# Kernel optimization log

Hardware: AMD Instinct MI355X
Metric: run time of the kernel (lower is better)

## Reference

```python
import jax, jax.numpy as jnp
import numpy as np

B, T, C = 8, 4096, 256
N_LAYER, LAYER_ID = 12, 5


def setup_inputs() -> dict:
    key = jax.random.key(0)
    ks = jax.random.split(key, 5)
    x = jax.random.normal(ks[0], (B, T, C), dtype=jnp.float32)
    scale = 1.0 / np.sqrt(C)
    Wk = jax.random.normal(ks[1], (C, C), jnp.float32) * scale
    Wv = jax.random.normal(ks[2], (C, C), jnp.float32) * scale
    Wr = jax.random.normal(ks[3], (C, C), jnp.float32) * scale
    Wo = jax.random.normal(ks[4], (C, C), jnp.float32) * scale
    # 'fancy' init from _init_weights
    ratio_0_to_1 = LAYER_ID / (N_LAYER - 1)
    h = np.arange(C, dtype=np.float64)
    decay = -5.0 + 8.0 * (h / (C - 1)) ** (0.7 + 1.3 * ratio_0_to_1)
    zigzag = ((np.arange(C) + 1) % 3 - 1) * 0.5
    first = np.log(0.3) + zigzag
    return dict(
        x=x, Wk=Wk, Wv=Wv, Wr=Wr, Wo=Wo,
        spatial_decay=jnp.asarray(decay, jnp.float32),
        spatial_first=jnp.asarray(first, jnp.float32),
        ln_w=jnp.ones((C,), jnp.float32),
        ln_b=jnp.zeros((C,), jnp.float32),
    )


def _wkv(w, u, k, v):
    # Numerically-stable RWKV WKV scan, matching wkv_cuda forward.
    # w, u: [C] (already divided by T); k, v: [B, T, C]. Returns y: [B, T, C].
    MIN_VALUE = -1e38

    def step(carry, kv):
        p, q, o = carry            # [B, C] each
        kt, vt = kv                # [B, C]
        no = jnp.maximum(o, u + kt)
        a = jnp.exp(o - no)
        b = jnp.exp(u + kt - no)
        y = (a * p + b * vt) / (a * q + b)
        no2 = jnp.maximum(w + o, kt)
        a2 = jnp.exp(w + o - no2)
        b2 = jnp.exp(kt - no2)
        return (a2 * p + b2 * vt, a2 * q + b2, no2), y

    p0 = jnp.zeros(k.shape[0:1] + k.shape[2:3], k.dtype)  # [B, C]
    q0 = jnp.zeros_like(p0)
    o0 = jnp.full_like(p0, MIN_VALUE)
    kT = jnp.swapaxes(k, 0, 1)  # [T, B, C]
    vT = jnp.swapaxes(v, 0, 1)
    _, yT = jax.lax.scan(step, (p0, q0, o0), (kT, vT))
    return jnp.swapaxes(yT, 0, 1)


def _layernorm(x, w, b, eps=1e-5):
    mu = jnp.mean(x, axis=-1, keepdims=True)
    xc = x - mu
    var = jnp.mean(xc * xc, axis=-1, keepdims=True)
    return xc * jax.lax.rsqrt(var + eps) * w + b


def reference(x, Wk, Wv, Wr, Wo, spatial_decay, spatial_first, ln_w, ln_b):
    # shift_pixel == 0 -> xk = xv = xr = x (module's own code path)
    t = x.shape[1]
    k = jnp.einsum('btc,dc->btd', x, Wk)
    v = jnp.einsum('btc,dc->btd', x, Wv)
    r = jnp.einsum('btc,dc->btd', x, Wr)
    sr = jax.nn.sigmoid(r)
    y = _wkv(spatial_decay / t, spatial_first / t, k, v)
    y = _layernorm(y, ln_w, ln_b)
    return jnp.einsum('btc,dc->btd', sr * y, Wo)
```

## Files before the change

### kernel.cpp

```cpp
#include <hip/hip_runtime.h>
#include <cstdint>
#include <cstddef>

#define B_ 8
#define T_ 4096
#define C_ 256
#define NC_ 256
#define L_ (T_ / NC_)
#define M_ (B_ * T_)

typedef float f32x4 __attribute__((ext_vector_type(4)));
typedef short bf16x8 __attribute__((ext_vector_type(8)));

__device__ __forceinline__ unsigned short f2b(float f) {
    unsigned int u = __float_as_uint(f);
    u += 0x7fffu + ((u >> 16) & 1u);
    return (unsigned short)(u >> 16);
}
__device__ __forceinline__ float b2f(unsigned short h) {
    return __uint_as_float(((unsigned int)h) << 16);
}

__global__ __launch_bounds__(256) void cvt_all(const float* __restrict__ x,
                                               const float* __restrict__ Wk,
                                               const float* __restrict__ Wv,
                                               const float* __restrict__ Wr,
                                               const float* __restrict__ Wo,
                                               unsigned short* __restrict__ xb,
                                               unsigned short* __restrict__ wb) {
    const int bid = blockIdx.x;
    const float* src;
    unsigned short* dst;
    size_t base;
    if (bid < 4096) {
        src = x; dst = xb;
        base = (size_t)bid * 2048;
    } else {
        const int r = bid - 4096;
        const int mat = r >> 5;
        src = (mat == 0) ? Wk : (mat == 1) ? Wv : (mat == 2) ? Wr : Wo;
        dst = wb + (size_t)mat * 65536;
        base = (size_t)(r & 31) * 2048;
    }
    const size_t i = base + (size_t)threadIdx.x * 8;
    float4 a = *(const float4*)(src + i);
    float4 b = *(const float4*)(src + i + 4);
    bf16x8 o;
    o[0] = (short)f2b(a.x); o[1] = (short)f2b(a.y);
    o[2] = (short)f2b(a.z); o[3] = (short)f2b(a.w);
    o[4] = (short)f2b(b.x); o[5] = (short)f2b(b.y);
    o[6] = (short)f2b(b.z); o[7] = (short)f2b(b.w);
    *(bf16x8*)(dst + i) = o;
}

__global__ __launch_bounds__(256, 3) void gemm_qkv(const unsigned short* __restrict__ A,
                                                   const unsigned short* __restrict__ w0,
                                                   const unsigned short* __restrict__ w1,
                                                   const unsigned short* __restrict__ w2,
                                                   float* __restrict__ f0,
                                                   float* __restrict__ f1,
                                                   unsigned short* __restrict__ b2) {
    __shared__ unsigned short wlds[64 * 264];
    __shared__ float stage[4][16 * 68];
    const int tid = threadIdx.x;
    const int wave = tid >> 6, lane = tid & 63;
    const int quad = lane >> 4, l16 = lane & 15;
    const int m0 = blockIdx.x * 64 + wave * 16;
    const int n0 = blockIdx.y * 64;
    float* myst = stage[wave];

    bf16x8 af[8];
    {
        const unsigned short* Ar = A + (size_t)(m0 + l16) * C_ + quad * 8;
#pragma unroll
        for (int kc = 0; kc < 8; ++kc) af[kc] = *(const bf16x8*)(Ar + kc * 32);
    }

    const int r = tid >> 5;
    const int cs = (tid & 31) * 8;

    bf16x8 tmp[8];
#pragma unroll
    for (int it = 0; it < 8; ++it)
        tmp[it] = *(const bf16x8*)(w0 + (size_t)(n0 + it * 8 + r) * C_ + cs);

    for (int mat = 0; mat < 3; ++mat) {
        __syncthreads();
#pragma unroll
        for (int it = 0; it < 8; ++it)
            *(bf16x8*)(wlds + (it * 8 + r) * 264 + cs) = tmp[it];
        __syncthreads();

        if (mat < 2) {
            const unsigned short* Wn = (mat == 0) ? w1 : w2;
#pragma unroll
            for (int it = 0; it < 8; ++it)
                tmp[it] = *(const bf16x8*)(Wn + (size_t)(n0 + it * 8 + r) * C_ + cs);
        }

        f32x4 acc[4];
#pragma unroll
        for (int nt = 0; nt < 4; ++nt) acc[nt] = (f32x4){0.f, 0.f, 0.f, 0.f};
#pragma unroll
        for (int nt = 0; nt < 4; ++nt) {
            const unsigned short* wrow = wlds + (nt * 16 + l16) * 264 + quad * 8;
#pragma unroll
            for (int kc = 0; kc < 8; ++kc) {
                bf16x8 wf = *(const bf16x8*)(wrow + kc * 32);
                acc[nt] = __builtin_amdgcn_mfma_f32_16x16x32_bf16(af[kc], wf, acc[nt], 0, 0, 0);
            }
        }

#pragma unroll
        for (int nt = 0; nt < 4; ++nt)
#pragma unroll
            for (int i = 0; i < 4; ++i)
                myst[(quad * 4 + i) * 68 + nt * 16 + l16] = acc[nt][i];
#pragma unroll
        for (int rr = 0; rr < 4; ++rr) {
            const int row = rr * 4 + quad;
            float4 t4 = *(const float4*)&myst[row * 68 + l16 * 4];
            const size_t gidx = (size_t)(m0 + row) * C_ + n0 + l16 * 4;
            if (mat == 0) {
                *(float4*)(f0 + gidx) = t4;
            } else if (mat == 1) {
                *(float4*)(f1 + gidx) = t4;
            } else {
                ushort4 s4;
                s4.x = f2b(1.f / (1.f + __expf(-t4.x)));
                s4.y = f2b(1.f / (1.f + __expf(-t4.y)));
                s4.z = f2b(1.f / (1.f + __expf(-t4.z)));
                s4.w = f2b(1.f / (1.f + __expf(-t4.w)));
                *(ushort4*)(b2 + gidx) = s4;
            }
        }
    }
}

__global__ __launch_bounds__(256, 3) void gemm_out(const unsigned short* __restrict__ A,
                                                   const unsigned short* __restrict__ w0,
                                                   float* __restrict__ f0) {
    __shared__ unsigned short wlds[64 * 264];
    __shared__ float stage[4][16 * 68];
    const int tid = threadIdx.x;
    const int wave = tid >> 6, lane = tid & 63;
    const int quad = lane >> 4, l16 = lane & 15;
    const int m0 = blockIdx.x * 64 + wave * 16;
    const int n0 = blockIdx.y * 64;
    float* myst = stage[wave];

    {
        const int r = tid >> 5;
        const int cs = (tid & 31) * 8;
        bf16x8 tmp[8];
#pragma unroll
        for (int it = 0; it < 8; ++it)
            tmp[it] = *(const bf16x8*)(w0 + (size_t)(n0 + it * 8 + r) * C_ + cs);
#pragma unroll
        for (int it = 0; it < 8; ++it)
            *(bf16x8*)(wlds + (it * 8 + r) * 264 + cs) = tmp[it];
    }
    __syncthreads();

    bf16x8 af[8];
    {
        const unsigned short* Ar = A + (size_t)(m0 + l16) * C_ + quad * 8;
#pragma unroll
        for (int kc = 0; kc < 8; ++kc) af[kc] = *(const bf16x8*)(Ar + kc * 32);
    }

    f32x4 acc[4];
#pragma unroll
    for (int nt = 0; nt < 4; ++nt) acc[nt] = (f32x4){0.f, 0.f, 0.f, 0.f};
#pragma unroll
    for (int nt = 0; nt < 4; ++nt) {
        const unsigned short* wrow = wlds + (nt * 16 + l16) * 264 + quad * 8;
#pragma unroll
        for (int kc = 0; kc < 8; ++kc) {
            bf16x8 wf = *(const bf16x8*)(wrow + kc * 32);
            acc[nt] = __builtin_amdgcn_mfma_f32_16x16x32_bf16(af[kc], wf, acc[nt], 0, 0, 0);
        }
    }

#pragma unroll
    for (int nt = 0; nt < 4; ++nt)
#pragma unroll
        for (int i = 0; i < 4; ++i)
            myst[(quad * 4 + i) * 68 + nt * 16 + l16] = acc[nt][i];
#pragma unroll
    for (int rr = 0; rr < 4; ++rr) {
        const int row = rr * 4 + quad;
        float4 t4 = *(const float4*)&myst[row * 68 + l16 * 4];
        *(float4*)(f0 + (size_t)(m0 + row) * C_ + n0 + l16 * 4) = t4;
    }
}

__global__ __launch_bounds__(256) void wkv_pass1(const float* __restrict__ k,
                                                 const float* __restrict__ v,
                                                 const float* __restrict__ decay,
                                                 float* __restrict__ sp, float* __restrict__ sq,
                                                 float* __restrict__ so) {
    const int c = threadIdx.x, chunk = blockIdx.x, b = blockIdx.y;
    const float w = decay[c] * (1.0f / T_);
    size_t base = ((size_t)b * T_ + (size_t)chunk * L_) * C_ + c;
    float p = 0.f, q = 0.f, o = -1e38f;
    for (int t = 0; t < L_; t += 8) {
        float kk[8], vv[8];
#pragma unroll
        for (int j = 0; j < 8; ++j) {
            kk[j] = k[base + (size_t)(t + j) * C_];
            vv[j] = v[base + (size_t)(t + j) * C_];
        }
#pragma unroll
        for (int j = 0; j < 8; ++j) {
            float wo = w + o;
            float no = fmaxf(wo, kk[j]);
            float a2 = __expf(wo - no), b2 = __expf(kk[j] - no);
            p = a2 * p + b2 * vv[j];
            q = a2 * q + b2;
            o = no;
        }
    }
    size_t idx = ((size_t)b * NC_ + chunk) * C_ + c;
    sp[idx] = p; sq[idx] = q; so[idx] = o;
}

__global__ __launch_bounds__(256) void wkv_combine_par(const float* __restrict__ decay,
                                                       float* __restrict__ sp,
                                                       float* __restrict__ sq,
                                                       float* __restrict__ so) {
    __shared__ float tp[16][17], tq[16][17], to[16][17];
    const int tid = threadIdx.x;
    const int cg = tid >> 4;
    const int cl = tid & 15;
    const int b = blockIdx.x;
    const int c = blockIdx.y * 16 + cl;
    const float wL = decay[c] * (1.0f / T_) * (float)L_;
    const float wL16 = wL * 16.0f;
    const size_t base = ((size_t)b * NC_ + (size_t)cg * 16) * C_ + c;

    float p = 0.f, q = 0.f, o = -1e38f;
#pragma unroll 4
    for (int j = 0; j < 16; ++j) {
        size_t idx = base + (size_t)j * C_;
        float lp = sp[idx], lq = sq[idx], lo = so[idx];
        float ow = o + wL;
        float no = fmaxf(ow, lo);
        float ea = __expf(ow - no), eb = __expf(lo - no);
        p = ea * p + eb * lp;
        q = ea * q + eb * lq;
        o = no;
    }
    tp[cg][cl] = p; tq[cg][cl] = q; to[cg][cl] = o;

    float ip = p, iq = q, io = o;
#pragma unroll
    for (int off = 1; off < 16; off <<= 1) {
        __syncthreads();
        float ap = 0.f, aq = 0.f, ao = 0.f;
        const bool doit = (cg >= off);
        if (doit) { ap = tp[cg - off][cl]; aq = tq[cg - off][cl]; ao = to[cg - off][cl]; }
        __syncthreads();
        if (doit) {
            float ow = ao + (float)off * wL16;
            float no = fmaxf(ow, io);
            float ea = __expf(ow - no), eb = __expf(io - no);
            ip = ea * ap + eb * ip;
            iq = ea * aq + eb * iq;
            io = no;
            tp[cg][cl] = ip; tq[cg][cl] = iq; to[cg][cl] = io;
        }
    }
    __syncthreads();

    float ep, eq, eo;
    if (cg == 0) { ep = 0.f; eq = 0.f; eo = -1e38f; }
    else         { ep = tp[cg - 1][cl]; eq = tq[cg - 1][cl]; eo = to[cg - 1][cl]; }

    for (int j = 0; j < 16; ++j) {
        size_t idx = base + (size_t)j * C_;
        float lp = sp[idx], lq = sq[idx], lo = so[idx];
        sp[idx] = ep; sq[idx] = eq; so[idx] = eo;
        float ow = eo + wL;
        float no = fmaxf(ow, lo);
        float ea = __expf(ow - no), eb = __expf(lo - no);
        ep = ea * ep + eb * lp;
        eq = ea * eq + eb * lq;
        eo = no;
    }
}

__global__ __launch_bounds__(256, 8) void wkv_pass2_ln(const float* __restrict__ k,
                                                       const float* __restrict__ v,
                                                       const unsigned short* __restrict__ sr,
                                                       const float* __restrict__ decay,
                                                       const float* __restrict__ first,
                                                       const float* __restrict__ lw,
                                                       const float* __restrict__ lb,
                                                       const float* __restrict__ sp,
                                                       const float* __restrict__ sq,
                                                       const float* __restrict__ so,
                                                       unsigned short* __restrict__ z) {
    __shared__ float tile[16][264];
    __shared__ float mu_s[16], rs_s[16];
    const int c = threadIdx.x, chunk = blockIdx.x, b = blockIdx.y;
    const int wave = c >> 6, lane = c & 63;
    const float w = decay[c] * (1.0f / T_);
    const float u = first[c] * (1.0f / T_);
    const float gw = lw[c], gb = lb[c];
    size_t sidx = ((size_t)b * NC_ + chunk) * C_ + c;
    float p = sp[sidx], q = sq[sidx], o = so[sidx];
    size_t base = ((size_t)b * T_ + (size_t)chunk * L_) * C_ + c;

    for (int t = 0; t < L_; t += 8) {
        float kk[8], vv[8];
#pragma unroll
        for (int j = 0; j < 8; ++j) {
            kk[j] = k[base + (size_t)(t + j) * C_];
            vv[j] = v[base + (size_t)(t + j) * C_];
        }
#pragma unroll
        for (int j = 0; j < 8; ++j) {
            float uk = u + kk[j];
            float no = fmaxf(o, uk);
            float a = __expf(o - no), bb = __expf(uk - no);
            tile[t + j][c] = (a * p + bb * vv[j]) / (a * q + bb);
            float wo = w + o;
            float no2 = fmaxf(wo, kk[j]);
            float a2 = __expf(wo - no2), b2 = __expf(kk[j] - no2);
            p = a2 * p + b2 * vv[j];
            q = a2 * q + b2;
            o = no2;
        }
    }
    __syncthreads();
#pragma unroll
    for (int r = 0; r < 4; ++r) {
        const int j = wave * 4 + r;
        float4 t4 = *(const float4*)&tile[j][lane * 4];
        float s = t4.x + t4.y + t4.z + t4.w;
        float ss = t4.x * t4.x + t4.y * t4.y + t4.z * t4.z + t4.w * t4.w;
#pragma unroll
        for (int m = 1; m < 64; m <<= 1) {
            s += __shfl_xor(s, m, 64);
            ss += __shfl_xor(ss, m, 64);
        }
        if (lane == 0) {
            float mu = s * (1.f / C_);
            mu_s[j] = mu;
            rs_s[j] = rsqrtf(ss * (1.f / C_) - mu * mu + 1e-5f);
        }
    }
    __syncthreads();
#pragma unroll
    for (int j = 0; j < L_; ++j) {
        float zz = (tile[j][c] - mu_s[j]) * rs_s[j] * gw + gb;
        zz *= b2f(sr[base + (size_t)j * C_]);
        z[base + (size_t)j * C_] = f2b(zz);
    }
}

extern "C" void kernel_launch(void* const* d_in, const int* in_sizes, int n_in,
                              void* d_out, int out_size, void* d_ws, size_t ws_size,
                              hipStream_t stream) {
    const float* x     = (const float*)d_in[0];
    const float* Wk    = (const float*)d_in[1];
    const float* Wv    = (const float*)d_in[2];
    const float* Wr    = (const float*)d_in[3];
    const float* Wo    = (const float*)d_in[4];
    const float* decay = (const float*)d_in[5];
    const float* first = (const float*)d_in[6];
    const float* lnw   = (const float*)d_in[7];
    const float* lnb   = (const float*)d_in[8];
    float* out = (float*)d_out;

    char* ws = (char*)d_ws;
    const size_t NE = (size_t)M_ * C_;
    unsigned short* wb  = (unsigned short*)ws; ws += 4 * 65536 * 2;
    unsigned short* xb  = (unsigned short*)ws; ws += NE * 2;
    float* kbuf = (float*)ws; ws += NE * 4;
    float* vbuf = (float*)ws; ws += NE * 4;
    unsigned short* srb = (unsigned short*)ws; ws += NE * 2;
    unsigned short* zb  = (unsigned short*)ws; ws += NE * 2;
    const size_t SE = (size_t)B_ * NC_ * C_;
    float* sp = (float*)ws; ws += SE * 4;
    float* sq = (float*)ws; ws += SE * 4;
    float* so = (float*)ws; ws += SE * 4;
    unsigned short* wkb = wb;
    unsigned short* wvb = wb + 65536;
    unsigned short* wrb = wb + 2 * 65536;
    unsigned short* wob = wb + 3 * 65536;

    cvt_all<<<4096 + 128, 256, 0, stream>>>(x, Wk, Wv, Wr, Wo, xb, wb);

    gemm_qkv<<<dim3(M_ / 64, 4), 256, 0, stream>>>(xb, wkb, wvb, wrb,
                                                   kbuf, vbuf, srb);

    wkv_pass1<<<dim3(NC_, B_), 256, 0, stream>>>(kbuf, vbuf, decay, sp, sq, so);
    wkv_combine_par<<<dim3(B_, C_ / 16), 256, 0, stream>>>(decay, sp, sq, so);
    wkv_pass2_ln<<<dim3(NC_, B_), 256, 0, stream>>>(kbuf, vbuf, srb, decay, first,
                                                    lnw, lnb, sp, sq, so, zb);

    gemm_out<<<dim3(M_ / 64, 4), 256, 0, stream>>>(zb, wob, out);
}
```

Baseline: 171.7 us.

## Fuse WKV chunk-state pass into QKV GEMM epilogue

Each wave's 16-row by 64-channel tile of K and V, which matches one 16-step WKV chunk, is kept in registers from the LDS staging buffer. The per-chunk (p, q, o) state is then computed directly in the GEMM epilogue. This removes the separate wkv_pass1 kernel, its launch, and its re-read of the K and V buffers from global memory. In exchange it adds registers and a serial exp chain to the GEMM kernel, which may lower occupancy under launch_bounds(256,3).

```diff
diff --git a/kernel.cpp b/kernel.cpp
--- a/kernel.cpp
+++ b/kernel.cpp
@@ -57,9 +57,13 @@
                                                    const unsigned short* __restrict__ w0,
                                                    const unsigned short* __restrict__ w1,
                                                    const unsigned short* __restrict__ w2,
+                                                   const float* __restrict__ decay,
                                                    float* __restrict__ f0,
                                                    float* __restrict__ f1,
-                                                   unsigned short* __restrict__ b2) {
+                                                   unsigned short* __restrict__ b2,
+                                                   float* __restrict__ sp,
+                                                   float* __restrict__ sq,
+                                                   float* __restrict__ so) {
     __shared__ unsigned short wlds[64 * 264];
     __shared__ float stage[4][16 * 68];
     const int tid = threadIdx.x;
@@ -83,6 +87,8 @@
 #pragma unroll
     for (int it = 0; it < 8; ++it)
         tmp[it] = *(const bf16x8*)(w0 + (size_t)(n0 + it * 8 + r) * C_ + cs);
+
+    float kreg[16], vreg[16];
 
     for (int mat = 0; mat < 3; ++mat) {
         __syncthreads();
@@ -134,6 +140,30 @@
                 *(ushort4*)(b2 + gidx) = s4;
             }
         }
+
+        if (mat == 0) {
+#pragma unroll
+            for (int j = 0; j < L_; ++j) kreg[j] = myst[j * 68 + lane];
+        } else if (mat == 1) {
+#pragma unroll
+            for (int j = 0; j < L_; ++j) vreg[j] = myst[j * 68 + lane];
+            const int ch = n0 + lane;
+            const float w = decay[ch] * (1.0f / T_);
+            float p = 0.f, q = 0.f, o = -1e38f;
+#pragma unroll
+            for (int j = 0; j < L_; ++j) {
+                float wo = w + o;
+                float no = fmaxf(wo, kreg[j]);
+                float a2 = __expf(wo - no), b2s = __expf(kreg[j] - no);
+                p = a2 * p + b2s * vreg[j];
+                q = a2 * q + b2s;
+                o = no;
+            }
+            const int bb = m0 / T_;
+            const int chunk = (m0 % T_) / L_;
+            const size_t idx = ((size_t)bb * NC_ + chunk) * C_ + ch;
+            sp[idx] = p; sq[idx] = q; so[idx] = o;
+        }
     }
 }
 
@@ -195,49 +225,19 @@
     }
 }
 
-__global__ __launch_bounds__(256) void wkv_pass1(const float* __restrict__ k,
-                                                 const float* __restrict__ v,
-                                                 const float* __restrict__ decay,
-                                                 float* __restrict__ sp, float* __restrict__ sq,
-                                                 float* __restrict__ so) {
-    const int c = threadIdx.x, chunk = blockIdx.x, b = blockIdx.y;
-    const float w = decay[c] * (1.0f / T_);
-    size_t base = ((size_t)b * T_ + (size_t)chunk * L_) * C_ + c;
-    float p = 0.f, q = 0.f, o = -1e38f;
-    for (int t = 0; t < L_; t += 8) {
-        float kk[8], vv[8];
-#pragma unroll
-        for (int j = 0; j < 8; ++j) {
-            kk[j] = k[base + (size_t)(t + j) * C_];
-            vv[j] = v[base + (size_t)(t + j) * C_];
-        }
-#pragma unroll
-        for (int j = 0; j < 8; ++j) {
-            float wo = w + o;
-            float no = fmaxf(wo, kk[j]);
-            float a2 = __expf(wo - no), b2 = __expf(kk[j] - no);
-            p = a2 * p + b2 * vv[j];
-            q = a2 * q + b2;
-            o = no;
-        }
-    }
-    size_t idx = ((size_t)b * NC_ + chunk) * C_ + c;
-    sp[idx] = p; sq[idx] = q; so[idx] = o;
-}
-
 __global__ __launch_bounds__(256) void wkv_combine_par(const float* __restrict__ decay,
                                                        float* __restrict__ sp,
                                                        float* __restrict__ sq,
                                                        float* __restrict__ so) {
     __shared__ float tp[16][17], tq[16][17], to[16][17];
     const int tid = threadIdx.x;
-    const int cg = tid >> 4;
+    const int cgi = tid >> 4;
     const int cl = tid & 15;
     const int b = blockIdx.x;
     const int c = blockIdx.y * 16 + cl;
     const float wL = decay[c] * (1.0f / T_) * (float)L_;
     const float wL16 = wL * 16.0f;
-    const size_t base = ((size_t)b * NC_ + (size_t)cg * 16) * C_ + c;
+    const size_t base = ((size_t)b * NC_ + (size_t)cgi * 16) * C_ + c;
 
     float p = 0.f, q = 0.f, o = -1e38f;
 #pragma unroll 4
@@ -251,15 +251,15 @@
         q = ea * q + eb * lq;
         o = no;
     }
-    tp[cg][cl] = p; tq[cg][cl] = q; to[cg][cl] = o;
+    tp[cgi][cl] = p; tq[cgi][cl] = q; to[cgi][cl] = o;
 
     float ip = p, iq = q, io = o;
 #pragma unroll
     for (int off = 1; off < 16; off <<= 1) {
         __syncthreads();
         float ap = 0.f, aq = 0.f, ao = 0.f;
-        const bool doit = (cg >= off);
-        if (doit) { ap = tp[cg - off][cl]; aq = tq[cg - off][cl]; ao = to[cg - off][cl]; }
+        const bool doit = (cgi >= off);
+        if (doit) { ap = tp[cgi - off][cl]; aq = tq[cgi - off][cl]; ao = to[cgi - off][cl]; }
         __syncthreads();
         if (doit) {
             float ow = ao + (float)off * wL16;
@@ -268,14 +268,14 @@
             ip = ea * ap + eb * ip;
             iq = ea * aq + eb * iq;
             io = no;
-            tp[cg][cl] = ip; tq[cg][cl] = iq; to[cg][cl] = io;
+            tp[cgi][cl] = ip; tq[cgi][cl] = iq; to[cgi][cl] = io;
         }
     }
     __syncthreads();
 
     float ep, eq, eo;
-    if (cg == 0) { ep = 0.f; eq = 0.f; eo = -1e38f; }
-    else         { ep = tp[cg - 1][cl]; eq = tq[cg - 1][cl]; eo = to[cg - 1][cl]; }
+    if (cgi == 0) { ep = 0.f; eq = 0.f; eo = -1e38f; }
+    else          { ep = tp[cgi - 1][cl]; eq = tq[cgi - 1][cl]; eo = to[cgi - 1][cl]; }
 
     for (int j = 0; j < 16; ++j) {
         size_t idx = base + (size_t)j * C_;
@@ -393,10 +393,9 @@
 
     cvt_all<<<4096 + 128, 256, 0, stream>>>(x, Wk, Wv, Wr, Wo, xb, wb);
 
-    gemm_qkv<<<dim3(M_ / 64, 4), 256, 0, stream>>>(xb, wkb, wvb, wrb,
-                                                   kbuf, vbuf, srb);
-
-    wkv_pass1<<<dim3(NC_, B_), 256, 0, stream>>>(kbuf, vbuf, decay, sp, sq, so);
+    gemm_qkv<<<dim3(M_ / 64, 4), 256, 0, stream>>>(xb, wkb, wvb, wrb, decay,
+                                                   kbuf, vbuf, srb, sp, sq, so);
+
     wkv_combine_par<<<dim3(B_, C_ / 16), 256, 0, stream>>>(decay, sp, sq, so);
     wkv_pass2_ln<<<dim3(NC_, B_), 256, 0, stream>>>(kbuf, vbuf, srb, decay, first,
                                                     lnw, lnb, sp, sq, so, zb);
```

Result: faster. 168.3 us (-2.0%).
